# Kernel optimization log

Hardware: AMD Instinct MI355X
Metric: run time of the kernel (lower is better)

## Reference

```python
import jax, jax.numpy as jnp
import numpy as np

B, T, M, D, H, DK, DV = 2, 1024, 1024, 1024, 16, 64, 64
R = 2 * T + M  # number of relative positions required by rel_shift path


def setup_inputs() -> dict:
    key = jax.random.key(0)
    ks = jax.random.split(key, 11)
    s = 0.02
    return {
        "inputs": jax.random.normal(ks[0], (B, T, D), jnp.float32),
        "attention_mask": jnp.ones((B, T, M + T), jnp.float32),
        "positional_encodings": jax.random.normal(ks[1], (R, D), jnp.float32),
        "memory": jax.random.normal(ks[2], (B, M, D), jnp.float32),
        "Wq": jax.random.normal(ks[3], (D, H * DK), jnp.float32) * s,
        "Wk": jax.random.normal(ks[4], (D, H * DK), jnp.float32) * s,
        "Wv": jax.random.normal(ks[5], (D, H * DV), jnp.float32) * s,
        "Wr": jax.random.normal(ks[6], (D, H * DK), jnp.float32) * s,
        "r_w_bias": jax.random.normal(ks[7], (H, DK), jnp.float32) * s,
        "r_r_bias": jax.random.normal(ks[8], (H, DK), jnp.float32) * s,
        "W_out": jax.random.normal(ks[9], (H * DV, D), jnp.float32) * s,
    }


def _rel_shift(m, attention_length):
    # m: [T_q, T_q + L] -> [T_q, L], TXL relative shift via reshape/slice
    tq, total = m.shape
    x = m.reshape(total, tq)[1:].reshape(tq, total - 1)
    return x[:, :attention_length]


def reference(inputs, attention_mask, positional_encodings, memory,
              Wq, Wk, Wv, Wr, r_w_bias, r_r_bias, W_out):
    b, t, d = inputs.shape
    values = jnp.concatenate([memory, inputs], axis=1)  # [B, L, D]
    L = values.shape[1]
    q = (inputs @ Wq).reshape(b, t, H, DK)
    k = (values @ Wk).reshape(b, L, H, DK)
    v = (values @ Wv).reshape(b, L, H, DV)
    rk = (positional_encodings @ Wr).reshape(-1, H, DK)  # [R, H, DK]
    # content + relative logits (TXL)
    content = jnp.einsum('bthd,bThd->bhtT', q + r_w_bias, k)        # [B,H,T,L]
    rel = jnp.einsum('bthd,rhd->bhtr', q + r_r_bias, rk)            # [B,H,T,R]
    rel = jax.vmap(jax.vmap(lambda m: _rel_shift(m, L)))(rel)       # [B,H,T,L]
    logits = (content + rel) * (DK ** -0.5)
    masked = logits - (1.0 - attention_mask[:, None, :, :]) * 1e30
    w = jax.nn.softmax(masked, axis=-1)
    attn = jnp.einsum('bhtT,bThd->bthd', w, v)                      # [B,T,H,DV]
    return attn.reshape(b, t, H * DV) @ W_out
```

## Files before the change

kernel.cpp:

```cpp
#include <hip/hip_runtime.h>
#include <hip/hip_fp16.h>
#include <stdint.h>

#define Bz 2
#define Tq 1024
#define Mm 1024
#define Hh 16
#define Ll 2048
#define Rr 3072

typedef __attribute__((ext_vector_type(8))) short bf16x8;
typedef __attribute__((ext_vector_type(4))) float f32x4;

typedef __attribute__((address_space(3))) uint8_t lds_u8_t;
typedef __attribute__((address_space(1))) uint8_t glb_u8_t;

__device__ __forceinline__ void gl2lds16(const void* g, void* l) {
  __builtin_amdgcn_global_load_lds((const glb_u8_t*)g, (lds_u8_t*)l, 16, 0, 0);
}

__device__ __forceinline__ unsigned short f2bf(float f) {
  unsigned int u = __builtin_bit_cast(unsigned int, f);
  u = u + 0x7fffu + ((u >> 16) & 1u);
  return (unsigned short)(u >> 16);
}
__device__ __forceinline__ float b2f(unsigned short s) {
  unsigned int u = ((unsigned int)s) << 16;
  return __builtin_bit_cast(float, u);
}

__global__ __launch_bounds__(256) void k_prep(const float* __restrict__ x,
                                              const float* __restrict__ mem,
                                              const float* __restrict__ pos,
                                              const float* __restrict__ mask,
                                              unsigned short* __restrict__ vin,
                                              unsigned short* __restrict__ pb,
                                              unsigned short* __restrict__ mb) {
  int bid = blockIdx.x;
  if (bid < 4096) {
    int idx = bid * 256 + threadIdx.x;
    int e = idx << 2;
    int row = e >> 10, col = e & 1023;
    int b = row >> 11, l = row & 2047;
    const float* s = (l < Mm) ? (mem + (((size_t)b * Mm + l) << 10) + col)
                              : (x + (((size_t)b * Tq + (l - Mm)) << 10) + col);
    float4 v = *(const float4*)s;
    ushort4 o;
    o.x = f2bf(v.x); o.y = f2bf(v.y); o.z = f2bf(v.z); o.w = f2bf(v.w);
    *(ushort4*)(vin + e) = o;
  } else if (bid < 7168) {
    int idx = (bid - 4096) * 256 + threadIdx.x;
    int e = idx << 2;
    float4 v = *(const float4*)(pos + e);
    ushort4 t;
    t.x = f2bf(v.x); t.y = f2bf(v.y); t.z = f2bf(v.z); t.w = f2bf(v.w);
    *(ushort4*)(pb + e) = t;
  } else {
    int idx = (bid - 7168) * 256 + threadIdx.x;
    int e = idx << 2;
    const float BIGM = 1.442695e30f;
    float4 v = *(const float4*)(mask + e);
    ushort4 t;
    t.x = f2bf((1.0f - v.x) * BIGM); t.y = f2bf((1.0f - v.y) * BIGM);
    t.z = f2bf((1.0f - v.z) * BIGM); t.w = f2bf((1.0f - v.w) * BIGM);
    *(ushort4*)(mb + e) = t;
  }
}

__global__ __launch_bounds__(256) void k_wtall(
    const float* __restrict__ w0, const float* __restrict__ w1,
    const float* __restrict__ w2, const float* __restrict__ w3,
    const float* __restrict__ w4,
    unsigned short* __restrict__ t0, unsigned short* __restrict__ t1,
    unsigned short* __restrict__ t2, unsigned short* __restrict__ t3,
    unsigned short* __restrict__ t4) {
  const float* W;
  unsigned short* WT;
  switch (blockIdx.z) {
    case 0: W = w0; WT = t0; break;
    case 1: W = w1; WT = t1; break;
    case 2: W = w2; WT = t2; break;
    case 3: W = w3; WT = t3; break;
    default: W = w4; WT = t4; break;
  }
  __shared__ float tile[64][65];
  int k0 = blockIdx.x * 64, n0 = blockIdx.y * 64;
  int tid = threadIdx.x;
  int rr = tid >> 4, c4 = (tid & 15) * 4;
#pragma unroll
  for (int it = 0; it < 4; ++it) {
    int r = rr + it * 16;
    float4 v = *(const float4*)(W + (size_t)(k0 + r) * 1024 + n0 + c4);
    tile[r][c4] = v.x; tile[r][c4 + 1] = v.y;
    tile[r][c4 + 2] = v.z; tile[r][c4 + 3] = v.w;
  }
  __syncthreads();
#pragma unroll
  for (int it = 0; it < 4; ++it) {
    int n = rr + it * 16;
    ushort4 o;
    o.x = f2bf(tile[c4 + 0][n]); o.y = f2bf(tile[c4 + 1][n]);
    o.z = f2bf(tile[c4 + 2][n]); o.w = f2bf(tile[c4 + 3][n]);
    *(ushort4*)(WT + (size_t)(n0 + n) * 1024 + k0 + c4) = o;
  }
}

template <int RMAP>
__device__ __forceinline__ void gemm_core(const unsigned short* __restrict__ A,
                                          const unsigned short* __restrict__ Bt,
                                          int m0, int n0, unsigned short* As,
                                          unsigned short* Bs, f32x4 acc[4][4]) {
  const int tid = threadIdx.x;
  const int w = tid >> 6, lane = tid & 63;
  const int quad = lane >> 4, li = lane & 15;
  const int wr = w >> 1, wc = w & 1;
  f32x4 z = {0.f, 0.f, 0.f, 0.f};
#pragma unroll
  for (int mi = 0; mi < 4; ++mi)
#pragma unroll
    for (int ni = 0; ni < 4; ++ni) acc[mi][ni] = z;

  const int rs = lane >> 2;
  const int cs = lane & 3;

  for (int k0 = 0; k0 < 1024; k0 += 32) {
    __syncthreads();
#pragma unroll
    for (int s = 0; s < 2; ++s) {
      int i = w * 2 + s;
      int r = i * 16 + rs;
      int c = cs ^ ((r >> 1) & 3);
      int ar = m0 + r;
      if (RMAP) ar = ar + 1024 + (ar & 1024);
      gl2lds16(A + (size_t)ar * 1024 + k0 + c * 8, (char*)As + i * 1024);
      int br = n0 + r;
      gl2lds16(Bt + (size_t)br * 1024 + k0 + c * 8, (char*)Bs + i * 1024);
    }
    __syncthreads();
    bf16x8 af[4], bfr[4];
#pragma unroll
    for (int mi = 0; mi < 4; ++mi) {
      int r = wr * 64 + mi * 16 + li;
      int ch = quad ^ ((r >> 1) & 3);
      af[mi] = *(const bf16x8*)((const char*)As + r * 64 + ch * 16);
    }
#pragma unroll
    for (int ni = 0; ni < 4; ++ni) {
      int r = wc * 64 + ni * 16 + li;
      int ch = quad ^ ((r >> 1) & 3);
      bfr[ni] = *(const bf16x8*)((const char*)Bs + r * 64 + ch * 16);
    }
#pragma unroll
    for (int mi = 0; mi < 4; ++mi)
#pragma unroll
      for (int ni = 0; ni < 4; ++ni)
        acc[mi][ni] = __builtin_amdgcn_mfma_f32_16x16x32_bf16(
            af[mi], bfr[ni], acc[mi][ni], 0, 0, 0);
  }
}

__global__ __launch_bounds__(256) void k_proj(
    const unsigned short* __restrict__ Vin, const unsigned short* __restrict__ Pb,
    const unsigned short* __restrict__ WqT, const unsigned short* __restrict__ WkT,
    const unsigned short* __restrict__ WvT, const unsigned short* __restrict__ WrT,
    const float* __restrict__ rwb, const float* __restrict__ rrb,
    unsigned short* __restrict__ qwb, unsigned short* __restrict__ qrb,
    unsigned short* __restrict__ kb, unsigned short* __restrict__ vtb,
    unsigned short* __restrict__ rkb) {
  __shared__ unsigned short As[128 * 32];
  __shared__ unsigned short Bs[128 * 32];
  const int t = blockIdx.x;
  const int tid = threadIdx.x, w = tid >> 6, lane = tid & 63;
  const int quad = lane >> 4, li = lane & 15, wr = w >> 1, wc = w & 1;
  f32x4 acc[4][4];

  if (t < 256) {
    int m0 = (t >> 3) * 128, n0 = (t & 7) * 128;
    gemm_core<0>(Vin, WkT, m0, n0, As, Bs, acc);
#pragma unroll
    for (int mi = 0; mi < 4; ++mi)
#pragma unroll
      for (int ni = 0; ni < 4; ++ni)
#pragma unroll
        for (int reg = 0; reg < 4; ++reg) {
          int rrow = m0 + wr * 64 + mi * 16 + quad * 4 + reg;
          int cc = n0 + wc * 64 + ni * 16 + li;
          kb[(size_t)rrow * 1024 + cc] = f2bf(acc[mi][ni][reg]);
        }
  } else if (t < 512) {
    int tt = t - 256;
    int m0 = (tt >> 3) * 128, n0 = (tt & 7) * 128;
    gemm_core<0>(Vin, WvT, m0, n0, As, Bs, acc);
#pragma unroll
    for (int mi = 0; mi < 4; ++mi)
#pragma unroll
      for (int ni = 0; ni < 4; ++ni) {
        int r0 = m0 + wr * 64 + mi * 16 + quad * 4;
        int b = r0 >> 11, l0 = r0 & 2047;
        int cc = n0 + wc * 64 + ni * 16 + li;
        ushort4 o;
        o.x = f2bf(acc[mi][ni][0]); o.y = f2bf(acc[mi][ni][1]);
        o.z = f2bf(acc[mi][ni][2]); o.w = f2bf(acc[mi][ni][3]);
        *(ushort4*)(vtb + ((size_t)(b * 1024 + cc)) * Ll + l0) = o;
      }
  } else if (t < 640) {
    int tt = t - 512;
    int m0 = (tt >> 3) * 128, n0 = (tt & 7) * 128;
    gemm_core<1>(Vin, WqT, m0, n0, As, Bs, acc);
#pragma unroll
    for (int mi = 0; mi < 4; ++mi)
#pragma unroll
      for (int ni = 0; ni < 4; ++ni) {
        int cc = n0 + wc * 64 + ni * 16 + li;
        float bw_ = rwb[cc], br_ = rrb[cc];
#pragma unroll
        for (int reg = 0; reg < 4; ++reg) {
          int rrow = m0 + wr * 64 + mi * 16 + quad * 4 + reg;
          size_t off = (size_t)rrow * 1024 + cc;
          qwb[off] = f2bf(acc[mi][ni][reg] + bw_);
          qrb[off] = f2bf(acc[mi][ni][reg] + br_);
        }
      }
  } else {
    int tt = t - 640;
    int m0 = (tt >> 3) * 128, n0 = (tt & 7) * 128;
    gemm_core<0>(Pb, WrT, m0, n0, As, Bs, acc);
#pragma unroll
    for (int mi = 0; mi < 4; ++mi)
#pragma unroll
      for (int ni = 0; ni < 4; ++ni)
#pragma unroll
        for (int reg = 0; reg < 4; ++reg) {
          int rrow = m0 + wr * 64 + mi * 16 + quad * 4 + reg;
          int cc = n0 + wc * 64 + ni * 16 + li;
          rkb[(size_t)rrow * 1024 + cc] = f2bf(acc[mi][ni][reg]);
        }
  }
}

__global__ __launch_bounds__(256) void k_gemm_out64(
    const unsigned short* __restrict__ attnb, const unsigned short* __restrict__ WoT,
    float* __restrict__ out) {
  __shared__ unsigned short As[64 * 32];
  __shared__ unsigned short Bs[128 * 32];
  int m0 = blockIdx.x * 64, n0 = blockIdx.y * 128;
  const int tid = threadIdx.x, w = tid >> 6, lane = tid & 63;
  const int quad = lane >> 4, li = lane & 15, wr = w >> 1, wc = w & 1;
  f32x4 z = {0.f, 0.f, 0.f, 0.f};
  f32x4 acc[2][4];
#pragma unroll
  for (int mi = 0; mi < 2; ++mi)
#pragma unroll
    for (int ni = 0; ni < 4; ++ni) acc[mi][ni] = z;
  const int rs = lane >> 2, cs = lane & 3;
  for (int k0 = 0; k0 < 1024; k0 += 32) {
    __syncthreads();
    {
      int r = w * 16 + rs;
      int c = cs ^ ((r >> 1) & 3);
      gl2lds16(attnb + (size_t)(m0 + r) * 1024 + k0 + c * 8, (char*)As + w * 1024);
    }
#pragma unroll
    for (int s = 0; s < 2; ++s) {
      int i = w * 2 + s;
      int r = i * 16 + rs;
      int c = cs ^ ((r >> 1) & 3);
      gl2lds16(WoT + (size_t)(n0 + r) * 1024 + k0 + c * 8, (char*)Bs + i * 1024);
    }
    __syncthreads();
    bf16x8 af[2], bfr[4];
#pragma unroll
    for (int mi = 0; mi < 2; ++mi) {
      int r = wr * 32 + mi * 16 + li;
      int ch = quad ^ ((r >> 1) & 3);
      af[mi] = *(const bf16x8*)((const char*)As + r * 64 + ch * 16);
    }
#pragma unroll
    for (int ni = 0; ni < 4; ++ni) {
      int r = wc * 64 + ni * 16 + li;
      int ch = quad ^ ((r >> 1) & 3);
      bfr[ni] = *(const bf16x8*)((const char*)Bs + r * 64 + ch * 16);
    }
#pragma unroll
    for (int mi = 0; mi < 2; ++mi)
#pragma unroll
      for (int ni = 0; ni < 4; ++ni)
        acc[mi][ni] = __builtin_amdgcn_mfma_f32_16x16x32_bf16(
            af[mi], bfr[ni], acc[mi][ni], 0, 0, 0);
  }
#pragma unroll
  for (int mi = 0; mi < 2; ++mi)
#pragma unroll
    for (int ni = 0; ni < 4; ++ni)
#pragma unroll
      for (int reg = 0; reg < 4; ++reg) {
        int rrow = m0 + wr * 32 + mi * 16 + quad * 4 + reg;
        int cc = n0 + wc * 64 + ni * 16 + li;
        out[(size_t)rrow * 1024 + cc] = acc[mi][ni][reg];
      }
}

__global__ __launch_bounds__(256, 3) void k_attn(
    const unsigned short* __restrict__ qw, const unsigned short* __restrict__ qr,
    const unsigned short* __restrict__ kb, const unsigned short* __restrict__ vt,
    const unsigned short* __restrict__ rkb, const unsigned short* __restrict__ mb,
    float* __restrict__ po, float* __restrict__ pl) {
  __shared__ unsigned short Ks[64 * 64];
  __shared__ unsigned short Vs[64 * 64];
  __shared__ unsigned short Rs[128 * 64];
  __shared__ unsigned short Sb[4][16 * 72];

  const int tid = threadIdx.x;
  const int w = tid >> 6, lane = tid & 63;
  const int quad = lane >> 4, li = lane & 15;
  const int qt = blockIdx.x, h = blockIdx.y;
  const int b = blockIdx.z >> 1, split = blockIdx.z & 1;
  const int t0blk = qt * 64;
  const int t0w = t0blk + w * 16;
  const int rboff = 48 - 16 * w;
  const int rbase0 = Tq - t0blk - 63 + (split << 10);

  bf16x8 aqw[2], aqr[2];
  {
    const unsigned short* p1 = qw + ((size_t)((b * Tq + t0w + li) * Hh + h)) * 64;
    aqw[0] = *(const bf16x8*)(p1 + quad * 8);
    aqw[1] = *(const bf16x8*)(p1 + 32 + quad * 8);
    const unsigned short* p2 = qr + ((size_t)((b * Tq + t0w + li) * Hh + h)) * 64;
    aqr[0] = *(const bf16x8*)(p2 + quad * 8);
    aqr[1] = *(const bf16x8*)(p2 + 32 + quad * 8);
  }

  f32x4 z = {0.f, 0.f, 0.f, 0.f};
  f32x4 o[4];
  o[0] = z; o[1] = z; o[2] = z; o[3] = z;
  f32x4 ol = z;

  const int srow = lane >> 3;
  const int scs = lane & 7;
  const float SC = 0.125f * 1.4426950408889634f;
  const short oneb = 0x3F80;
  const bf16x8 onesf = {oneb, oneb, oneb, oneb, oneb, oneb, oneb, oneb};

  unsigned short* pw = &Sb[w][0];
  const unsigned short* mrowA = mb + ((size_t)(b * Tq + t0w + li)) * Ll;
  int srcl[4];
#pragma unroll
  for (int reg = 0; reg < 4; ++reg) {
    int row = quad * 4 + reg;
    srcl[reg] = (lane & 48) + ((li + row + 1) & 15);
  }

  for (int jt = 0; jt < 16; ++jt) {
    const int j0 = (split << 10) + jt * 64;
    __syncthreads();
#pragma unroll
    for (int s = 0; s < 2; ++s) {
      int i = w * 2 + s;
      int r = i * 8 + srow;
      int c = scs ^ (r & 7);
      gl2lds16(kb + ((size_t)((b * Ll + j0 + r) * Hh + h)) * 64 + c * 8,
               (char*)Ks + i * 1024);
      gl2lds16(vt + ((size_t)((b * Hh + h) * 64 + r)) * Ll + j0 + c * 8,
               (char*)Vs + i * 1024);
    }
    if (jt == 0) {
#pragma unroll
      for (int s = 0; s < 4; ++s) {
        int i = w * 4 + s;
        int r = i * 8 + srow;
        int gr = rbase0 + r;
        if (gr > Rr - 1) gr = Rr - 1;
        int c = scs ^ (r & 7);
        gl2lds16(rkb + ((size_t)gr * Hh + h) * 64 + c * 8, (char*)Rs + i * 1024);
      }
    } else {
      int ph0 = (64 * (jt + 1)) & 127;
#pragma unroll
      for (int s = 0; s < 2; ++s) {
        int i2 = w * 2 + s;
        int rr = i2 * 8 + srow;
        int gr = rbase0 + 64 * jt + 64 + rr;
        if (gr > Rr - 1) gr = Rr - 1;
        int c = scs ^ (rr & 7);
        gl2lds16(rkb + ((size_t)gr * Hh + h) * 64 + c * 8,
                 (char*)Rs + ph0 * 128 + i2 * 1024);
      }
    }
    __syncthreads();

    f32x4 sc[4];
    sc[0] = z; sc[1] = z; sc[2] = z; sc[3] = z;
#pragma unroll
    for (int ks = 0; ks < 2; ++ks)
#pragma unroll
      for (int nt = 0; nt < 4; ++nt) {
        int j = nt * 16 + li;
        int ch = (ks * 4 + quad) ^ (j & 7);
        bf16x8 kf = *(const bf16x8*)((const char*)Ks + j * 128 + ch * 16);
        sc[nt] = __builtin_amdgcn_mfma_f32_16x16x32_bf16(aqw[ks], kf, sc[nt], 0, 0, 0);
      }
    f32x4 bd[5];
    bd[0] = z; bd[1] = z; bd[2] = z; bd[3] = z; bd[4] = z;
#pragma unroll
    for (int ks = 0; ks < 2; ++ks)
#pragma unroll
      for (int nt = 0; nt < 5; ++nt) {
        int pr = (rboff + nt * 16 + li + 64 * jt) & 127;
        int ch = (ks * 4 + quad) ^ (pr & 7);
        bf16x8 rf = *(const bf16x8*)((const char*)Rs + pr * 128 + ch * 16);
        bd[nt] = __builtin_amdgcn_mfma_f32_16x16x32_bf16(aqr[ks], rf, bd[nt], 0, 0, 0);
      }
    float rot[4][4];
#pragma unroll
    for (int nt = 0; nt < 4; ++nt)
#pragma unroll
      for (int reg = 0; reg < 4; ++reg)
        rot[nt][reg] = __shfl(sc[nt][reg], srcl[reg], 64);
#pragma unroll
    for (int nt = 0; nt < 5; ++nt)
#pragma unroll
      for (int reg = 0; reg < 4; ++reg) {
        int row = quad * 4 + reg;
        int jj = nt * 16 + li + row - 15;
        int ntlo = (nt == 0) ? 3 : (nt - 1);
        int nthi = (nt > 3) ? 0 : nt;
        float val = ((li + row) >= 15) ? rot[nthi][reg] : rot[ntlo][reg];
        float s = val + bd[nt][reg];
        if ((unsigned)jj < 64u)
          pw[row * 72 + jj] = __builtin_bit_cast(unsigned short, __float2half(s));
      }
    __builtin_amdgcn_s_waitcnt(0xc07f);

#pragma unroll
    for (int ks = 0; ks < 2; ++ks) {
      const int cofs = ks * 32 + quad * 8;
      ushort4 s0 = *(const ushort4*)(pw + li * 72 + cofs);
      ushort4 s1 = *(const ushort4*)(pw + li * 72 + cofs + 4);
      bf16x8 mv = *(const bf16x8*)(mrowA + j0 + cofs);
      unsigned short su[8] = {s0.x, s0.y, s0.z, s0.w, s1.x, s1.y, s1.z, s1.w};
      bf16x8 ap;
#pragma unroll
      for (int i2 = 0; i2 < 8; ++i2) {
        float sf = __half2float(__builtin_bit_cast(__half, su[i2]));
        float mvf = b2f((unsigned short)mv[i2]);
        float p = exp2f(sf * SC - mvf);
        ap[i2] = (short)f2bf(p);
      }
      ol = __builtin_amdgcn_mfma_f32_16x16x32_bf16(ap, onesf, ol, 0, 0, 0);
#pragma unroll
      for (int nt = 0; nt < 4; ++nt) {
        int dv = nt * 16 + li;
        int ch = (ks * 4 + quad) ^ (dv & 7);
        bf16x8 vf = *(const bf16x8*)((const char*)Vs + dv * 128 + ch * 16);
        o[nt] = __builtin_amdgcn_mfma_f32_16x16x32_bf16(ap, vf, o[nt], 0, 0, 0);
      }
    }
  }
  const int bs = (b * 2 + split) * 16 + h;
#pragma unroll
  for (int nt = 0; nt < 4; ++nt)
#pragma unroll
    for (int reg = 0; reg < 4; ++reg) {
      int trow = t0w + quad * 4 + reg;
      po[((size_t)bs * 1024 + trow) * 64 + nt * 16 + li] = o[nt][reg];
    }
  if (li == 0) {
#pragma unroll
    for (int reg = 0; reg < 4; ++reg) {
      int trow = t0w + quad * 4 + reg;
      pl[(size_t)bs * 1024 + trow] = ol[reg];
    }
  }
}

__global__ __launch_bounds__(256) void k_combine(
    const float* __restrict__ po, const float* __restrict__ pl,
    unsigned short* __restrict__ attnb) {
  int id = blockIdx.x * 256 + threadIdx.x;
  int dv4 = (id & 15) << 2;
  int t = (id >> 4) & 1023;
  int h = (id >> 14) & 15;
  int b = id >> 18;
  size_t r0 = ((size_t)((b * 2 + 0) * 16 + h)) * 1024 + t;
  size_t r1 = ((size_t)((b * 2 + 1) * 16 + h)) * 1024 + t;
  float inv = 1.0f / (pl[r0] + pl[r1]);
  float4 o0 = *(const float4*)(po + r0 * 64 + dv4);
  float4 o1 = *(const float4*)(po + r1 * 64 + dv4);
  ushort4 res;
  res.x = f2bf((o0.x + o1.x) * inv);
  res.y = f2bf((o0.y + o1.y) * inv);
  res.z = f2bf((o0.z + o1.z) * inv);
  res.w = f2bf((o0.w + o1.w) * inv);
  *(ushort4*)(attnb + ((size_t)(b * 1024 + t)) * 1024 + h * 64 + dv4) = res;
}

extern "C" void kernel_launch(void* const* d_in, const int* in_sizes, int n_in,
                              void* d_out, int out_size, void* d_ws, size_t ws_size,
                              hipStream_t stream) {
  const float* x = (const float*)d_in[0];
  const float* mask = (const float*)d_in[1];
  const float* pos = (const float*)d_in[2];
  const float* mem = (const float*)d_in[3];
  const float* Wq = (const float*)d_in[4];
  const float* Wk = (const float*)d_in[5];
  const float* Wv = (const float*)d_in[6];
  const float* Wr = (const float*)d_in[7];
  const float* rwb = (const float*)d_in[8];
  const float* rrb = (const float*)d_in[9];
  const float* Wo = (const float*)d_in[10];
  float* out = (float*)d_out;

  uint8_t* ws = (uint8_t*)d_ws;
  const size_t MB = 1024 * 1024;
  unsigned short* Vinb = (unsigned short*)(ws + 0);
  unsigned short* WqT = (unsigned short*)(ws + 8 * MB);
  unsigned short* WkT = (unsigned short*)(ws + 10 * MB);
  unsigned short* WvT = (unsigned short*)(ws + 12 * MB);
  unsigned short* WrT = (unsigned short*)(ws + 14 * MB);
  unsigned short* WoT = (unsigned short*)(ws + 16 * MB);
  unsigned short* Pb = (unsigned short*)(ws + 18 * MB);
  unsigned short* qwb = (unsigned short*)(ws + 24 * MB);
  unsigned short* qrb = (unsigned short*)(ws + 28 * MB);
  unsigned short* kb = (unsigned short*)(ws + 32 * MB);
  unsigned short* vtb = (unsigned short*)(ws + 40 * MB);
  unsigned short* rkb = (unsigned short*)(ws + 48 * MB);
  unsigned short* mbb = (unsigned short*)(ws + 54 * MB);
  float* po = (float*)(ws + 0);
  float* pl = (float*)(ws + 18 * MB);
  unsigned short* attnb = (unsigned short*)(ws + 19 * MB);

  hipLaunchKernelGGL(k_prep, dim3(11264), dim3(256), 0, stream,
                     x, mem, pos, mask, Vinb, Pb, mbb);
  hipLaunchKernelGGL(k_wtall, dim3(16, 16, 5), dim3(256), 0, stream,
                     Wq, Wk, Wv, Wr, Wo, WqT, WkT, WvT, WrT, WoT);
  hipLaunchKernelGGL(k_proj, dim3(832), dim3(256), 0, stream,
                     Vinb, Pb, WqT, WkT, WvT, WrT, rwb, rrb, qwb, qrb, kb, vtb, rkb);
  hipLaunchKernelGGL(k_attn, dim3(16, 16, 4), dim3(256), 0, stream,
                     qwb, qrb, kb, vtb, rkb, mbb, po, pl);
  hipLaunchKernelGGL(k_combine, dim3(2048), dim3(256), 0, stream, po, pl, attnb);
  hipLaunchKernelGGL(k_gemm_out64, dim3(32, 8), dim3(256), 0, stream,
                     attnb, WoT, out);
}
```

Baseline: 268.8 us.

## Drop split-K in attention, double-buffer K/V/R tiles, fuse combine

The attention kernel no longer splits the key range across two blocks. Each block now walks all 32 key tiles and normalizes its output directly, which removes the partial-output buffers and the separate combine kernel. K/V tiles are double-buffered and the R ring is widened to 256 rows, so the next tile's global-to-LDS loads overlap the current tile's compute with one barrier per iteration. The trade-off is half as many blocks (512), a higher LDS footprint, and an occupancy hint lowered from 3 to 2. Together these may leave the GPU underfilled.

```diff
diff --git a/kernel.cpp b/kernel.cpp
--- a/kernel.cpp
+++ b/kernel.cpp
@@ -300,25 +300,24 @@
       }
 }
 
-__global__ __launch_bounds__(256, 3) void k_attn(
+__global__ __launch_bounds__(256, 2) void k_attn(
     const unsigned short* __restrict__ qw, const unsigned short* __restrict__ qr,
     const unsigned short* __restrict__ kb, const unsigned short* __restrict__ vt,
     const unsigned short* __restrict__ rkb, const unsigned short* __restrict__ mb,
-    float* __restrict__ po, float* __restrict__ pl) {
-  __shared__ unsigned short Ks[64 * 64];
-  __shared__ unsigned short Vs[64 * 64];
-  __shared__ unsigned short Rs[128 * 64];
+    unsigned short* __restrict__ attnb) {
+  __shared__ unsigned short Ks[2][64 * 64];
+  __shared__ unsigned short Vs[2][64 * 64];
+  __shared__ unsigned short Rs[256 * 64];
   __shared__ unsigned short Sb[4][16 * 72];
 
   const int tid = threadIdx.x;
   const int w = tid >> 6, lane = tid & 63;
   const int quad = lane >> 4, li = lane & 15;
-  const int qt = blockIdx.x, h = blockIdx.y;
-  const int b = blockIdx.z >> 1, split = blockIdx.z & 1;
+  const int qt = blockIdx.x, h = blockIdx.y, b = blockIdx.z;
   const int t0blk = qt * 64;
   const int t0w = t0blk + w * 16;
   const int rboff = 48 - 16 * w;
-  const int rbase0 = Tq - t0blk - 63 + (split << 10);
+  const int rbase0 = Tq - t0blk - 63;
 
   bf16x8 aqw[2], aqr[2];
   {
@@ -350,44 +349,57 @@
     srcl[reg] = (lane & 48) + ((li + row + 1) & 15);
   }
 
-  for (int jt = 0; jt < 16; ++jt) {
-    const int j0 = (split << 10) + jt * 64;
+#pragma unroll
+  for (int s = 0; s < 4; ++s) {
+    int i = w * 4 + s;
+    int r = i * 8 + srow;
+    int gr = rbase0 + r;
+    if (gr > Rr - 1) gr = Rr - 1;
+    int c = scs ^ (r & 7);
+    gl2lds16(rkb + ((size_t)gr * Hh + h) * 64 + c * 8, (char*)Rs + i * 1024);
+  }
+#pragma unroll
+  for (int s = 0; s < 2; ++s) {
+    int i = w * 2 + s;
+    int r = i * 8 + srow;
+    int c = scs ^ (r & 7);
+    gl2lds16(kb + ((size_t)((b * Ll + r) * Hh + h)) * 64 + c * 8,
+             (char*)Ks[0] + i * 1024);
+    gl2lds16(vt + ((size_t)((b * Hh + h) * 64 + r)) * Ll + c * 8,
+             (char*)Vs[0] + i * 1024);
+  }
+
+  for (int jt = 0; jt < 32; ++jt) {
+    const int j0 = jt * 64;
+    const int cur = jt & 1, nxt = cur ^ 1;
+    __builtin_amdgcn_s_waitcnt(0x0F70);
     __syncthreads();
-#pragma unroll
-    for (int s = 0; s < 2; ++s) {
-      int i = w * 2 + s;
-      int r = i * 8 + srow;
-      int c = scs ^ (r & 7);
-      gl2lds16(kb + ((size_t)((b * Ll + j0 + r) * Hh + h)) * 64 + c * 8,
-               (char*)Ks + i * 1024);
-      gl2lds16(vt + ((size_t)((b * Hh + h) * 64 + r)) * Ll + j0 + c * 8,
-               (char*)Vs + i * 1024);
-    }
-    if (jt == 0) {
-#pragma unroll
-      for (int s = 0; s < 4; ++s) {
-        int i = w * 4 + s;
+    if (jt < 31) {
+      const int j0n = j0 + 64;
+#pragma unroll
+      for (int s = 0; s < 2; ++s) {
+        int i = w * 2 + s;
         int r = i * 8 + srow;
-        int gr = rbase0 + r;
-        if (gr > Rr - 1) gr = Rr - 1;
         int c = scs ^ (r & 7);
-        gl2lds16(rkb + ((size_t)gr * Hh + h) * 64 + c * 8, (char*)Rs + i * 1024);
-      }
-    } else {
-      int ph0 = (64 * (jt + 1)) & 127;
+        gl2lds16(kb + ((size_t)((b * Ll + j0n + r) * Hh + h)) * 64 + c * 8,
+                 (char*)Ks[nxt] + i * 1024);
+        gl2lds16(vt + ((size_t)((b * Hh + h) * 64 + r)) * Ll + j0n + c * 8,
+                 (char*)Vs[nxt] + i * 1024);
+      }
 #pragma unroll
       for (int s = 0; s < 2; ++s) {
         int i2 = w * 2 + s;
         int rr = i2 * 8 + srow;
-        int gr = rbase0 + 64 * jt + 64 + rr;
+        int ofs = j0 + 128 + rr;
+        int gr = rbase0 + ofs;
         if (gr > Rr - 1) gr = Rr - 1;
+        int ring = ofs & 255;
         int c = scs ^ (rr & 7);
-        gl2lds16(rkb + ((size_t)gr * Hh + h) * 64 + c * 8,
-                 (char*)Rs + ph0 * 128 + i2 * 1024);
-      }
-    }
-    __syncthreads();
-
+        gl2lds16(rkb + ((size_t)gr * Hh + h) * 64 + c * 8, (char*)Rs + ring * 128);
+      }
+    }
+    const unsigned short* KsC = Ks[cur];
+    const unsigned short* VsC = Vs[cur];
     f32x4 sc[4];
     sc[0] = z; sc[1] = z; sc[2] = z; sc[3] = z;
 #pragma unroll
@@ -396,7 +408,7 @@
       for (int nt = 0; nt < 4; ++nt) {
         int j = nt * 16 + li;
         int ch = (ks * 4 + quad) ^ (j & 7);
-        bf16x8 kf = *(const bf16x8*)((const char*)Ks + j * 128 + ch * 16);
+        bf16x8 kf = *(const bf16x8*)((const char*)KsC + j * 128 + ch * 16);
         sc[nt] = __builtin_amdgcn_mfma_f32_16x16x32_bf16(aqw[ks], kf, sc[nt], 0, 0, 0);
       }
     f32x4 bd[5];
@@ -405,7 +417,7 @@
     for (int ks = 0; ks < 2; ++ks)
 #pragma unroll
       for (int nt = 0; nt < 5; ++nt) {
-        int pr = (rboff + nt * 16 + li + 64 * jt) & 127;
+        int pr = (rboff + nt * 16 + li + j0) & 255;
         int ch = (ks * 4 + quad) ^ (pr & 7);
         bf16x8 rf = *(const bf16x8*)((const char*)Rs + pr * 128 + ch * 16);
         bd[nt] = __builtin_amdgcn_mfma_f32_16x16x32_bf16(aqr[ks], rf, bd[nt], 0, 0, 0);
@@ -430,7 +442,6 @@
           pw[row * 72 + jj] = __builtin_bit_cast(unsigned short, __float2half(s));
       }
     __builtin_amdgcn_s_waitcnt(0xc07f);
-
 #pragma unroll
     for (int ks = 0; ks < 2; ++ks) {
       const int cofs = ks * 32 + quad * 8;
@@ -451,47 +462,22 @@
       for (int nt = 0; nt < 4; ++nt) {
         int dv = nt * 16 + li;
         int ch = (ks * 4 + quad) ^ (dv & 7);
-        bf16x8 vf = *(const bf16x8*)((const char*)Vs + dv * 128 + ch * 16);
+        bf16x8 vf = *(const bf16x8*)((const char*)VsC + dv * 128 + ch * 16);
         o[nt] = __builtin_amdgcn_mfma_f32_16x16x32_bf16(ap, vf, o[nt], 0, 0, 0);
       }
     }
   }
-  const int bs = (b * 2 + split) * 16 + h;
+  float inv[4];
+#pragma unroll
+  for (int reg = 0; reg < 4; ++reg) inv[reg] = 1.0f / ol[reg];
 #pragma unroll
   for (int nt = 0; nt < 4; ++nt)
 #pragma unroll
     for (int reg = 0; reg < 4; ++reg) {
       int trow = t0w + quad * 4 + reg;
-      po[((size_t)bs * 1024 + trow) * 64 + nt * 16 + li] = o[nt][reg];
-    }
-  if (li == 0) {
-#pragma unroll
-    for (int reg = 0; reg < 4; ++reg) {
-      int trow = t0w + quad * 4 + reg;
-      pl[(size_t)bs * 1024 + trow] = ol[reg];
-    }
-  }
-}
-
-__global__ __launch_bounds__(256) void k_combine(
-    const float* __restrict__ po, const float* __restrict__ pl,
-    unsigned short* __restrict__ attnb) {
-  int id = blockIdx.x * 256 + threadIdx.x;
-  int dv4 = (id & 15) << 2;
-  int t = (id >> 4) & 1023;
-  int h = (id >> 14) & 15;
-  int b = id >> 18;
-  size_t r0 = ((size_t)((b * 2 + 0) * 16 + h)) * 1024 + t;
-  size_t r1 = ((size_t)((b * 2 + 1) * 16 + h)) * 1024 + t;
-  float inv = 1.0f / (pl[r0] + pl[r1]);
-  float4 o0 = *(const float4*)(po + r0 * 64 + dv4);
-  float4 o1 = *(const float4*)(po + r1 * 64 + dv4);
-  ushort4 res;
-  res.x = f2bf((o0.x + o1.x) * inv);
-  res.y = f2bf((o0.y + o1.y) * inv);
-  res.z = f2bf((o0.z + o1.z) * inv);
-  res.w = f2bf((o0.w + o1.w) * inv);
-  *(ushort4*)(attnb + ((size_t)(b * 1024 + t)) * 1024 + h * 64 + dv4) = res;
+      attnb[((size_t)(b * Tq + trow)) * 1024 + h * 64 + nt * 16 + li] =
+          f2bf(o[nt][reg] * inv[reg]);
+    }
 }
 
 extern "C" void kernel_launch(void* const* d_in, const int* in_sizes, int n_in,
@@ -525,8 +511,6 @@
   unsigned short* vtb = (unsigned short*)(ws + 40 * MB);
   unsigned short* rkb = (unsigned short*)(ws + 48 * MB);
   unsigned short* mbb = (unsigned short*)(ws + 54 * MB);
-  float* po = (float*)(ws + 0);
-  float* pl = (float*)(ws + 18 * MB);
   unsigned short* attnb = (unsigned short*)(ws + 19 * MB);
 
   hipLaunchKernelGGL(k_prep, dim3(11264), dim3(256), 0, stream,
@@ -535,9 +519,8 @@
                      Wq, Wk, Wv, Wr, Wo, WqT, WkT, WvT, WrT, WoT);
   hipLaunchKernelGGL(k_proj, dim3(832), dim3(256), 0, stream,
                      Vinb, Pb, WqT, WkT, WvT, WrT, rwb, rrb, qwb, qrb, kb, vtb, rkb);
-  hipLaunchKernelGGL(k_attn, dim3(16, 16, 4), dim3(256), 0, stream,
-                     qwb, qrb, kb, vtb, rkb, mbb, po, pl);
-  hipLaunchKernelGGL(k_combine, dim3(2048), dim3(256), 0, stream, po, pl, attnb);
+  hipLaunchKernelGGL(k_attn, dim3(16, 16, 2), dim3(256), 0, stream,
+                     qwb, qrb, kb, vtb, rkb, mbb, attnb);
   hipLaunchKernelGGL(k_gemm_out64, dim3(32, 8), dim3(256), 0, stream,
                      attnb, WoT, out);
 }
```

Result: no change. 268.3 us (-0.2%).
